# Kernel optimization log

Hardware: AMD Instinct MI355X
Metric: run time of the kernel (lower is better)

## Reference

```python
import jax, jax.numpy as jnp
import numpy as np


def setup_inputs() -> dict:
    key = jax.random.key(0)
    k1, k2, k3, k4 = jax.random.split(key, 4)
    B, C_in, C_out, H, W = 8, 256, 256, 160, 160
    mask = jax.random.randint(k1, (B, 1, H, W), 0, 2, dtype=jnp.int32)  # binary hard mask
    ori = jax.random.normal(k2, (B, C_in, H, W), dtype=jnp.float32)
    weight = jax.random.normal(k3, (C_out, C_in, 3, 3), dtype=jnp.float32) * 0.02
    bias = jax.random.normal(k4, (C_out,), dtype=jnp.float32) * 0.02
    return {"mask": mask, "ori": ori, "weight": weight, "bias": bias}


def reference(mask, ori, weight, bias):
    # apply_mask: broadcast binary [B,1,H,W] mask over channels, zero masked regions
    x = ori * mask.astype(ori.dtype)
    # dense 3x3 conv, stride 1, padding 1 (SAME) -> output [B, C_out, H, W]
    out = jax.lax.conv_general_dilated(
        x, weight,
        window_strides=(1, 1),
        padding='SAME',
        dimension_numbers=('NCHW', 'OIHW', 'NCHW'),
    )
    return out + bias[None, :, None, None]
```

## Files before the change

### kernel.cpp

```cpp
#include <hip/hip_runtime.h>

typedef __attribute__((ext_vector_type(8))) short short8;
typedef __attribute__((ext_vector_type(4))) float f32x4;

#define B_    8
#define CI    256
#define CO    256
#define Hh    160
#define Ww    160
#define HP    162
#define WP    162
#define HWp   (Hh * Ww)
#define XPAD_ELEMS (B_ * HP * WP * CI)
#define W2_ELEMS   (9 * CI * CO)
#define NT    36

__device__ __forceinline__ unsigned short f2bf(float f) {
  unsigned int u = __float_as_uint(f);
  u += 0x7FFFu + ((u >> 16) & 1u);
  return (unsigned short)(u >> 16);
}

__global__ void prep_w_kernel(const float* __restrict__ w, unsigned short* __restrict__ w2) {
  int i = blockIdx.x * 256 + threadIdx.x;
  if (i >= W2_ELEMS) return;
  int ci = i & 255;
  int t = i >> 8;
  int co = t & 255;
  int s = t >> 8;
  w2[i] = f2bf(w[(co * 256 + ci) * 9 + s]);
}

__global__ void zero_border(unsigned short* __restrict__ xp) {
  int g = blockIdx.x * 256 + threadIdx.x;
  int pos = g >> 5;
  int c = (g & 31) << 3;
  int n = pos / 644;
  int p = pos - n * 644;
  int y, x;
  if (p < 324) { y = (p < 162) ? 0 : 161; x = (p < 162) ? p : p - 162; }
  else { int q = p - 324; y = 1 + (q >> 1); x = (q & 1) ? 161 : 0; }
  unsigned short* d = xp + (((size_t)(n * 162 + y)) * 162 + x) * 256 + c;
  *(uint4*)d = (uint4){0u, 0u, 0u, 0u};
}

__global__ void prep_x_kernel(const float* __restrict__ ori, const int* __restrict__ mask,
                              unsigned short* __restrict__ xp) {
  int bid = blockIdx.x;
  int wt = bid % 3;
  int t1 = bid / 3;
  int cit = t1 & 3;
  int t2 = t1 >> 2;
  int h = t2 % Hh;
  int n = t2 / Hh;
  int t = threadIdx.x;

  __shared__ float tile[64][65];

  int wl = t & 63;
  int w = wt * 64 + wl;
  bool valid = (w < Ww);
  float m = 0.f;
  if (valid) m = (float)mask[(n * Hh + h) * Ww + w];
  const float* src = ori + (((size_t)(n * CI + cit * 64) * Hh + h) * Ww + w);
  int r0 = t >> 6;
#pragma unroll
  for (int k = 0; k < 16; ++k) {
    int ci_l = r0 * 16 + k;
    float v = 0.f;
    if (valid) v = src[(size_t)ci_l * HWp] * m;
    tile[ci_l][wl] = v;
  }
  __syncthreads();

  int wl2 = t >> 2;
  int wo = wt * 64 + wl2;
  if (wo < Ww) {
    int cseg = (t & 3) * 16;
    union { unsigned short u[8]; uint4 v; } p0, p1;
#pragma unroll
    for (int j = 0; j < 8; ++j) p0.u[j] = f2bf(tile[cseg + j][wl2]);
#pragma unroll
    for (int j = 0; j < 8; ++j) p1.u[j] = f2bf(tile[cseg + 8 + j][wl2]);
    unsigned short* dst = xp + ((size_t)((n * HP + h + 1) * WP) + (wo + 1)) * CI + cit * 64 + cseg;
    *(uint4*)dst = p0.v;
    *(uint4*)(dst + 8) = p1.v;
  }
}

__device__ __forceinline__ void gload16(const unsigned short* g, unsigned short* l) {
  __builtin_amdgcn_global_load_lds((const __attribute__((address_space(1))) void*)g,
                                   (__attribute__((address_space(3))) void*)l, 16, 0, 0);
}

__global__ void __launch_bounds__(512, 2) sconv_gemm(const unsigned short* __restrict__ xp,
                                                     const unsigned short* __restrict__ w2,
                                                     const float* __restrict__ bias,
                                                     float* __restrict__ out) {
  __shared__ unsigned short lds[2][26624];

  const int bid = blockIdx.x;
  const int n = bid & 7;
  const int h = bid >> 3;

  const int t = threadIdx.x;
  const int l = t & 63;
  const int wv = t >> 6;
  const int wm = wv & 3;
  const int wn = wv >> 2;

  const int lr = l >> 3;
  const int lane_stage = (wv * 8 + lr) * 256 + (((l & 7) ^ lr) << 3);
  const unsigned xrow_base = (unsigned)(n * HP + h) * WP;

  const int lc = l & 15;
  const int cs0 = (((l >> 4)) ^ (l & 7)) << 3;
  const int cs1 = ((4 + (l >> 4)) ^ (l & 7)) << 3;

  f32x4 acc[4][5];
#pragma unroll
  for (int mi = 0; mi < 4; ++mi)
#pragma unroll
    for (int ni = 0; ni < 5; ++ni)
      acc[mi][ni] = (f32x4){0.f, 0.f, 0.f, 0.f};

  auto STAGE = [&](int tt) {
    int shift = tt >> 2;
    int kh = shift / 3;
    int kw = shift - kh * 3;
    int ci0 = (tt & 3) << 6;
    const unsigned short* ag = w2 + shift * (CI * CO) + ci0 + lane_stage;
    const unsigned short* bg = xp + ((size_t)(xrow_base + kh * WP + kw) << 8) + ci0 + lane_stage;
    unsigned short* sa = &lds[tt & 1][0];
    unsigned short* sb = &lds[tt & 1][16384];
#pragma unroll
    for (int r = 0; r < 4; ++r)
      gload16(ag + r * 16384, sa + (r * 64 + wv * 8) * 64);
#pragma unroll
    for (int r = 0; r < 2; ++r)
      gload16(bg + r * 16384, sb + (r * 64 + wv * 8) * 64);
    if (wv < 4)
      gload16(bg + 32768, sb + (128 + wv * 8) * 64);
  };

  STAGE(0);
  STAGE(1);
  asm volatile("s_waitcnt vmcnt(6)" ::: "memory");
  __builtin_amdgcn_s_barrier();

  for (int tt = 0; tt < NT; ++tt) {
    const unsigned short* Ab = &lds[tt & 1][0];
    const unsigned short* Bb = &lds[tt & 1][16384];

    short8 bf[5][2];
#pragma unroll
    for (int ni = 0; ni < 5; ++ni) {
      const unsigned short* br = Bb + (wn * 80 + ni * 16 + lc) * 64;
      bf[ni][0] = *(const short8*)(br + cs0);
      bf[ni][1] = *(const short8*)(br + cs1);
    }
#pragma unroll
    for (int mi = 0; mi < 4; ++mi) {
      const unsigned short* ar = Ab + (wm * 64 + mi * 16 + lc) * 64;
      short8 a0 = *(const short8*)(ar + cs0);
      short8 a1 = *(const short8*)(ar + cs1);
      __builtin_amdgcn_s_setprio(1);
#pragma unroll
      for (int ni = 0; ni < 5; ++ni) {
        acc[mi][ni] = __builtin_amdgcn_mfma_f32_16x16x32_bf16(a0, bf[ni][0], acc[mi][ni], 0, 0, 0);
        acc[mi][ni] = __builtin_amdgcn_mfma_f32_16x16x32_bf16(a1, bf[ni][1], acc[mi][ni], 0, 0, 0);
      }
      __builtin_amdgcn_s_setprio(0);
    }

    __syncthreads();
    if (tt + 2 < NT) STAGE(tt + 2);
  }

  const int co_l = (l >> 4) * 4;
#pragma unroll
  for (int mi = 0; mi < 4; ++mi) {
    int cobase = wm * 64 + mi * 16 + co_l;
    const float4 bv = *(const float4*)(bias + cobase);
    size_t obase = ((size_t)n * CO + cobase) * HWp + (size_t)h * Ww;
#pragma unroll
    for (int ni = 0; ni < 5; ++ni) {
      int w = wn * 80 + ni * 16 + lc;
      f32x4 v = acc[mi][ni];
      out[obase + w]             = v[0] + bv.x;
      out[obase + HWp + w]       = v[1] + bv.y;
      out[obase + 2 * HWp + w]   = v[2] + bv.z;
      out[obase + 3 * HWp + w]   = v[3] + bv.w;
    }
  }
}

extern "C" void kernel_launch(void* const* d_in, const int* in_sizes, int n_in,
                              void* d_out, int out_size, void* d_ws, size_t ws_size,
                              hipStream_t stream) {
  const int* mask = (const int*)d_in[0];
  const float* ori = (const float*)d_in[1];
  const float* weight = (const float*)d_in[2];
  const float* bias = (const float*)d_in[3];
  float* out = (float*)d_out;

  unsigned short* xp = (unsigned short*)d_ws;
  unsigned short* w2 = xp + XPAD_ELEMS;

  zero_border<<<644, 256, 0, stream>>>(xp);
  prep_w_kernel<<<(W2_ELEMS + 255) / 256, 256, 0, stream>>>(weight, w2);
  prep_x_kernel<<<B_ * Hh * 4 * 3, 256, 0, stream>>>(ori, mask, xp);
  sconv_gemm<<<B_ * Hh, 512, 0, stream>>>(xp, w2, bias, out);
}
```

Measured before the change: 343.5 us.

## Load weights directly to registers in MFMA layout and restructure GEMM into quadrant phases

```diff
diff --git a/kernel.cpp b/kernel.cpp
--- a/kernel.cpp
+++ b/kernel.cpp
@@ -12,7 +12,7 @@
 #define WP    162
 #define HWp   (Hh * Ww)
 #define XPAD_ELEMS (B_ * HP * WP * CI)
-#define W2_ELEMS   (9 * CI * CO)
+#define W3_ELEMS   (9 * CI * CO)
 #define NT    36
 
 __device__ __forceinline__ unsigned short f2bf(float f) {
@@ -21,14 +21,15 @@
   return (unsigned short)(u >> 16);
 }
 
-__global__ void prep_w_kernel(const float* __restrict__ w, unsigned short* __restrict__ w2) {
+__global__ void prep_w_kernel(const float* __restrict__ w, unsigned short* __restrict__ w3) {
   int i = blockIdx.x * 256 + threadIdx.x;
-  if (i >= W2_ELEMS) return;
-  int ci = i & 255;
-  int t = i >> 8;
-  int co = t & 255;
-  int s = t >> 8;
-  w2[i] = f2bf(w[(co * 256 + ci) * 9 + s]);
+  if (i >= W3_ELEMS) return;
+  int e = i & 7, l = (i >> 3) & 63, g = i >> 9;
+  int mi = g & 1, wm = (g >> 1) & 3, kk = (g >> 3) & 1;
+  int qm = (g >> 4) & 1, cic = (g >> 5) & 3, shift = g >> 7;
+  int co = qm * 128 + wm * 32 + mi * 16 + (l & 15);
+  int ci = cic * 64 + kk * 32 + (l >> 4) * 8 + e;
+  w3[i] = f2bf(w[(co * 256 + ci) * 9 + shift]);
 }
 
 __global__ void zero_border(unsigned short* __restrict__ xp) {
@@ -93,11 +94,10 @@
                                    (__attribute__((address_space(3))) void*)l, 16, 0, 0);
 }
 
-__global__ void __launch_bounds__(512, 2) sconv_gemm(const unsigned short* __restrict__ xp,
-                                                     const unsigned short* __restrict__ w2,
-                                                     const float* __restrict__ bias,
-                                                     float* __restrict__ out) {
-  __shared__ unsigned short lds[2][26624];
+__global__ void __launch_bounds__(256, 2)
+sconv_gemm(const unsigned short* __restrict__ xp, const unsigned short* __restrict__ w3,
+           const float* __restrict__ bias, float* __restrict__ out) {
+  __shared__ unsigned short Bs[4 * 5120];
 
   const int bid = blockIdx.x;
   const int n = bid & 7;
@@ -106,93 +106,123 @@
   const int t = threadIdx.x;
   const int l = t & 63;
   const int wv = t >> 6;
-  const int wm = wv & 3;
-  const int wn = wv >> 2;
 
   const int lr = l >> 3;
-  const int lane_stage = (wv * 8 + lr) * 256 + (((l & 7) ^ lr) << 3);
-  const unsigned xrow_base = (unsigned)(n * HP + h) * WP;
-
-  const int lc = l & 15;
-  const int cs0 = (((l >> 4)) ^ (l & 7)) << 3;
-  const int cs1 = ((4 + (l >> 4)) ^ (l & 7)) << 3;
-
-  f32x4 acc[4][5];
-#pragma unroll
-  for (int mi = 0; mi < 4; ++mi)
-#pragma unroll
-    for (int ni = 0; ni < 5; ++ni)
-      acc[mi][ni] = (f32x4){0.f, 0.f, 0.f, 0.f};
-
-  auto STAGE = [&](int tt) {
-    int shift = tt >> 2;
-    int kh = shift / 3;
-    int kw = shift - kh * 3;
-    int ci0 = (tt & 3) << 6;
-    const unsigned short* ag = w2 + shift * (CI * CO) + ci0 + lane_stage;
-    const unsigned short* bg = xp + ((size_t)(xrow_base + kh * WP + kw) << 8) + ci0 + lane_stage;
-    unsigned short* sa = &lds[tt & 1][0];
-    unsigned short* sb = &lds[tt & 1][16384];
-#pragma unroll
-    for (int r = 0; r < 4; ++r)
-      gload16(ag + r * 16384, sa + (r * 64 + wv * 8) * 64);
-#pragma unroll
-    for (int r = 0; r < 2; ++r)
-      gload16(bg + r * 16384, sb + (r * 64 + wv * 8) * 64);
-    if (wv < 4)
-      gload16(bg + 32768, sb + (128 + wv * 8) * 64);
+  const int swz8 = ((l & 7) ^ lr) << 3;
+  const int lc = l & 15, hi4 = l >> 4, lx7 = l & 7;
+  const unsigned xrow = (unsigned)(n * HP + h);
+
+  const int basej = (wv < 2) ? wv * 24 : 48 + (wv - 2) * 16;
+  const unsigned bof0 = (unsigned)(basej + 0 + lr) * 256 + swz8;
+  const unsigned bof1 = (unsigned)(basej + 8 + lr) * 256 + swz8;
+  const unsigned bof2 = (unsigned)(basej + 16 + lr) * 256 + swz8;
+
+  f32x4 acc[2][2][2][5];
+#pragma unroll
+  for (int a = 0; a < 2; ++a)
+#pragma unroll
+    for (int b = 0; b < 2; ++b)
+#pragma unroll
+      for (int c = 0; c < 2; ++c)
+#pragma unroll
+        for (int d = 0; d < 5; ++d)
+          acc[a][b][c][d] = (f32x4){0.f, 0.f, 0.f, 0.f};
+
+  auto STAGE_B = [&](int ts, int qn) {
+    int cic = (ts * 57) >> 9;
+    int sh = ts - cic * 9;
+    int kh = (sh * 11) >> 5;
+    int kw = sh - kh * 3;
+    const unsigned short* src = xp + (((size_t)(xrow + kh) * WP + kw + qn * 80) << 8) + (cic << 6);
+    unsigned short* dst = (unsigned short*)Bs + ((ts & 1) * 2 + qn) * 5120 + basej * 64;
+    gload16(src + bof0, dst);
+    gload16(src + bof1, dst + 512);
+    if (wv < 2) gload16(src + bof2, dst + 1024);
   };
 
-  STAGE(0);
-  STAGE(1);
-  asm volatile("s_waitcnt vmcnt(6)" ::: "memory");
-  __builtin_amdgcn_s_barrier();
-
-  for (int tt = 0; tt < NT; ++tt) {
-    const unsigned short* Ab = &lds[tt & 1][0];
-    const unsigned short* Bb = &lds[tt & 1][16384];
-
-    short8 bf[5][2];
-#pragma unroll
-    for (int ni = 0; ni < 5; ++ni) {
-      const unsigned short* br = Bb + (wn * 80 + ni * 16 + lc) * 64;
-      bf[ni][0] = *(const short8*)(br + cs0);
-      bf[ni][1] = *(const short8*)(br + cs1);
+  auto AG4 = [&](int ts, int qm, short8* r) {
+    int cic = (ts * 57) >> 9;
+    int sh = ts - cic * 9;
+    const unsigned short* p = w3 + (((size_t)(sh * 128 + cic * 32 + qm * 16 + wv * 2)) << 9) + (l << 3);
+    r[0] = *(const short8*)(p);
+    r[1] = *(const short8*)(p + 512);
+    r[2] = *(const short8*)(p + 4096);
+    r[3] = *(const short8*)(p + 4096 + 512);
+  };
+
+#define BRD(tb, qn, kk, ni) \
+  (*(const short8*)((unsigned short*)Bs + ((tb) * 2 + (qn)) * 5120 + \
+                    (((ni) * 16 + lc) * 64) + (((((kk) << 2) + hi4) ^ lx7) << 3)))
+
+#define PHASE(tb, qm, qn, AREG) do { \
+  _Pragma("unroll") \
+  for (int kk = 0; kk < 2; ++kk) { \
+    short8 bb[5]; \
+    _Pragma("unroll") \
+    for (int ni = 0; ni < 5; ++ni) bb[ni] = BRD(tb, qn, kk, ni); \
+    __builtin_amdgcn_s_setprio(1); \
+    _Pragma("unroll") \
+    for (int mi = 0; mi < 2; ++mi) \
+      _Pragma("unroll") \
+      for (int ni = 0; ni < 5; ++ni) \
+        acc[qm][mi][qn][ni] = __builtin_amdgcn_mfma_f32_16x16x32_bf16( \
+            AREG[kk * 2 + mi], bb[ni], acc[qm][mi][qn][ni], 0, 0, 0); \
+    __builtin_amdgcn_s_setprio(0); \
+  } \
+  asm volatile("s_waitcnt vmcnt(12)" ::: "memory"); \
+  asm volatile("s_barrier" ::: "memory"); \
+} while (0)
+
+  short8 a0A[4], a0B[4], aQ1[4];
+
+  STAGE_B(0, 0);
+  STAGE_B(0, 1);
+  STAGE_B(1, 0);
+  AG4(0, 0, a0A);
+  AG4(0, 1, aQ1);
+  asm volatile("s_waitcnt vmcnt(12)" ::: "memory");
+  asm volatile("s_barrier" ::: "memory");
+
+  for (int tt = 0; tt < NT; tt += 2) {
+    const bool n1 = (tt + 2 < NT);
+    const bool n2 = (tt + 3 < NT);
+    STAGE_B(tt + 1, 1);
+    PHASE(0, 0, 0, a0A);
+    PHASE(0, 1, 0, aQ1);
+    AG4(tt + 1, 0, a0B);
+    if (n1) STAGE_B(tt + 2, 0);
+    PHASE(0, 1, 1, aQ1);
+    AG4(tt + 1, 1, aQ1);
+    PHASE(0, 0, 1, a0A);
+    if (n1) STAGE_B(tt + 2, 1);
+    PHASE(1, 0, 0, a0B);
+    PHASE(1, 1, 0, aQ1);
+    if (n1) AG4(tt + 2, 0, a0A);
+    if (n2) STAGE_B(tt + 3, 0);
+    PHASE(1, 1, 1, aQ1);
+    if (n1) AG4(tt + 2, 1, aQ1);
+    PHASE(1, 0, 1, a0B);
+  }
+
+#pragma unroll
+  for (int qm = 0; qm < 2; ++qm)
+#pragma unroll
+    for (int mi = 0; mi < 2; ++mi) {
+      int cobase = qm * 128 + wv * 32 + mi * 16 + hi4 * 4;
+      const float4 bv = *(const float4*)(bias + cobase);
+      float* op = out + (((size_t)n * CO + cobase) * Hh + h) * Ww;
+#pragma unroll
+      for (int qn = 0; qn < 2; ++qn)
+#pragma unroll
+        for (int ni = 0; ni < 5; ++ni) {
+          int w = qn * 80 + ni * 16 + lc;
+          f32x4 v = acc[qm][mi][qn][ni];
+          op[w]                   = v[0] + bv.x;
+          op[(size_t)HWp + w]     = v[1] + bv.y;
+          op[(size_t)2 * HWp + w] = v[2] + bv.z;
+          op[(size_t)3 * HWp + w] = v[3] + bv.w;
+        }
     }
-#pragma unroll
-    for (int mi = 0; mi < 4; ++mi) {
-      const unsigned short* ar = Ab + (wm * 64 + mi * 16 + lc) * 64;
-      short8 a0 = *(const short8*)(ar + cs0);
-      short8 a1 = *(const short8*)(ar + cs1);
-      __builtin_amdgcn_s_setprio(1);
-#pragma unroll
-      for (int ni = 0; ni < 5; ++ni) {
-        acc[mi][ni] = __builtin_amdgcn_mfma_f32_16x16x32_bf16(a0, bf[ni][0], acc[mi][ni], 0, 0, 0);
-        acc[mi][ni] = __builtin_amdgcn_mfma_f32_16x16x32_bf16(a1, bf[ni][1], acc[mi][ni], 0, 0, 0);
-      }
-      __builtin_amdgcn_s_setprio(0);
-    }
-
-    __syncthreads();
-    if (tt + 2 < NT) STAGE(tt + 2);
-  }
-
-  const int co_l = (l >> 4) * 4;
-#pragma unroll
-  for (int mi = 0; mi < 4; ++mi) {
-    int cobase = wm * 64 + mi * 16 + co_l;
-    const float4 bv = *(const float4*)(bias + cobase);
-    size_t obase = ((size_t)n * CO + cobase) * HWp + (size_t)h * Ww;
-#pragma unroll
-    for (int ni = 0; ni < 5; ++ni) {
-      int w = wn * 80 + ni * 16 + lc;
-      f32x4 v = acc[mi][ni];
-      out[obase + w]             = v[0] + bv.x;
-      out[obase + HWp + w]       = v[1] + bv.y;
-      out[obase + 2 * HWp + w]   = v[2] + bv.z;
-      out[obase + 3 * HWp + w]   = v[3] + bv.w;
-    }
-  }
 }
 
 extern "C" void kernel_launch(void* const* d_in, const int* in_sizes, int n_in,
@@ -205,10 +235,10 @@
   float* out = (float*)d_out;
 
   unsigned short* xp = (unsigned short*)d_ws;
-  unsigned short* w2 = xp + XPAD_ELEMS;
+  unsigned short* w3 = xp + XPAD_ELEMS;
 
   zero_border<<<644, 256, 0, stream>>>(xp);
-  prep_w_kernel<<<(W2_ELEMS + 255) / 256, 256, 0, stream>>>(weight, w2);
+  prep_w_kernel<<<(W3_ELEMS + 255) / 256, 256, 0, stream>>>(weight, w3);
   prep_x_kernel<<<B_ * Hh * 4 * 3, 256, 0, stream>>>(ori, mask, xp);
-  sconv_gemm<<<B_ * Hh, 512, 0, stream>>>(xp, w2, bias, out);
-}
+  sconv_gemm<<<1280, 256, 0, stream>>>(xp, w3, bias, out);
+}
```

Measured after the change: 341.5 us. Within noise of the previous version (-0.6%).
